# Optimization experiments

Measured on AMD Instinct MI355X. Metric: run time of the kernel, lower is better.

Reference implementation:

```python
import jax, jax.numpy as jnp
import numpy as np

B, N, DIM = 4, 2048, 768
HEADS, DH, DEPTH = 12, 64, 4
W = 35                     # hard-coded window size
P = DIM // 2               # window-embedding proj dim
V4 = DIM // 4              # window-embedding value dim
PB = DIM // 4              # dynamic pos-bias MLP width
FF = DIM * 4
NEG = float(np.finfo(np.float32).max)


def setup_inputs() -> dict:
    key = jax.random.key(0)
    ks = iter(jax.random.split(key, 32))
    r = lambda shape: jax.random.normal(next(ks), shape, jnp.float32) * 0.02
    return dict(
        x=jax.random.normal(next(ks), (B, N, DIM), jnp.float32),
        mask=jnp.zeros((B, N), bool),
        ln1_g=jnp.ones((DEPTH, DIM)), ln1_b=jnp.zeros((DEPTH, DIM)),
        qkv_W=r((DEPTH, DIM, 3 * HEADS * DH)),
        temp=jnp.full((DEPTH,), 15.5, jnp.float32),
        we_lin_W=r((DEPTH, DIM, P)), we_q_W=r((DEPTH, P, P)),
        we_k_W=r((DEPTH, DIM, P)), we_v_W=r((DEPTH, DIM, V4)),
        we_bos=jnp.zeros((DEPTH, V4)), we_scale=jnp.ones((DEPTH,)),
        out_W=r((DEPTH, DIM + V4, DIM)),
        ln2_g=jnp.ones((DEPTH, DIM)), ln2_b=jnp.zeros((DEPTH, DIM)),
        glu_W=r((DEPTH, DIM, 2 * FF)), glu_b=jnp.zeros((DEPTH, 2 * FF)),
        ffo_W=r((DEPTH, FF, DIM)), ffo_b=jnp.zeros((DEPTH, DIM)),
        pb_W1=r((1, PB)), pb_b1=jnp.zeros((PB,)),
        pb_W2=r((PB, PB)), pb_b2=jnp.zeros((PB,)),
        pb_W3=r((PB, HEADS)), pb_b3=jnp.zeros((HEADS,)),
    )


def _ln(x, g, b):
    m = x.mean(-1, keepdims=True)
    v = ((x - m) ** 2).mean(-1, keepdims=True)
    return (x - m) * jax.lax.rsqrt(v + 1e-5) * g + b


def _l2norm(t):
    # matches F.normalize(p=2, dim=-1): x / max(||x||, 1e-12)
    return t / jnp.maximum(jnp.linalg.norm(t, axis=-1, keepdims=True), 1e-12)


def _pos_bias(n, W1, b1, W2, b2, W3, b3):
    # DynamicPositionBias(dim=PB, depth=2): Linear->ReLU, Linear->ReLU, Linear
    pos = jnp.arange(-n + 1, n, dtype=jnp.float32)[:, None]          # (2n-1, 1)
    h = jax.nn.relu(pos @ W1 + b1)
    h = jax.nn.relu(h @ W2 + b2)
    out = h @ W3 + b3                                                # (2n-1, H)
    idx = jnp.arange(n)[:, None] - jnp.arange(n)[None, :] + n - 1    # (n, n)
    return jnp.transpose(out[idx], (2, 0, 1))                        # (H, n, n)


def _sinu(n, scale):
    # ScaledSinuEmbedding over proj dim P
    inv = 1.0 / (10000.0 ** (jnp.arange(0, P, 2, dtype=jnp.float32) / P))
    s = jnp.arange(n, dtype=jnp.float32)[:, None] * inv[None, :]
    return jnp.concatenate([jnp.sin(s), jnp.cos(s)], -1) * scale     # (n, P)


def _forward(x, mask, ln1_g, ln1_b, qkv_W, temp, we_lin_W, we_q_W, we_k_W,
             we_v_W, we_bos, we_scale, out_W, ln2_g, ln2_b, glu_W, glu_b,
             ffo_W, ffo_b, pb_W1, pb_b1, pb_W2, pb_b2, pb_W3, pb_b3):
    Bz, Nn, _ = x.shape
    pad = (-Nn) % W
    nw = (Nn + pad) // W
    bias = _pos_bias(W, pb_W1, pb_b1, pb_W2, pb_b2, pb_W3, pb_b3)    # (H, W, W)
    causal = jnp.triu(jnp.ones((W, W), bool), 1)
    mpad = jnp.concatenate([mask, jnp.ones((Bz, pad), bool)], 1).reshape(Bz, nw, W)
    valid = ~mpad                                                    # (B, w, n)
    amask = ~(valid[:, None, :, :, None] & valid[:, None, :, None, :]) | causal
    we_mask = mpad[:, :, None, :]                                    # (B, w, 1, n)
    lengths = jnp.maximum(valid.sum(-1), 1).astype(jnp.float32)[..., None, None]
    sinu35 = _sinu(W, 1.0)                                           # (W, P)

    for l in range(DEPTH):
        # ---- PreNorm + windowed cosine attention ----
        h = _ln(x, ln1_g[l], ln1_b[l])
        hp = jnp.concatenate([h, jnp.zeros((Bz, pad, DIM), h.dtype)], 1)
        hp = hp.reshape(Bz, nw, W, DIM)
        qkv = (hp @ qkv_W[l]).reshape(Bz, nw, W, HEADS, DH, 3)
        q, k, v = (jnp.transpose(qkv[..., i], (0, 3, 1, 2, 4)) for i in range(3))
        q, k = _l2norm(q), _l2norm(k)
        dots = jnp.einsum('bhwid,bhwjd->bhwij', q, k) * temp[l] + bias[None, :, None]
        dots = jnp.where(amask, -NEG, dots)
        attn = jax.nn.softmax(dots, axis=-1)
        o = jnp.einsum('bhwij,bhwjd->bhwid', attn, v)
        o = jnp.transpose(o, (0, 2, 3, 1, 4)).reshape(Bz, nw, W, HEADS * DH)
        # ---- window_embeddings: pooled prev-window embedding attention ----
        we = jnp.where(mpad[..., None], 0.0, o) @ we_lin_W[l]         # (B,w,n,P)
        we = jax.nn.relu(we.sum(-2, keepdims=True) / lengths)        # (B,w,1,P)
        wq = we @ we_q_W[l]
        k2 = o @ we_k_W[l] + sinu35 * we_scale[l]
        v2 = o @ we_v_W[l]
        d2 = jnp.einsum('bwid,bwjd->bwij', wq, k2) * (P ** -0.5)
        d2 = jnp.where(we_mask, -NEG, d2)
        o2 = jnp.einsum('bwij,bwjd->bwid', jax.nn.softmax(d2, -1), v2)  # (B,w,1,V4)
        bos = jnp.broadcast_to(we_bos[l], (Bz, 1, 1, V4))
        o2 = jnp.concatenate([bos, o2], 1)[:, :-1]                   # shift by one window
        o = jnp.concatenate([o, jnp.broadcast_to(o2, (Bz, nw, W, V4))], -1)
        o = (o @ out_W[l]).reshape(Bz, nw * W, DIM)[:, :Nn]
        x = x + o
        # ---- PreNorm + GLU feed-forward ----
        h2 = _ln(x, ln2_g[l], ln2_b[l])
        a, g = jnp.split(h2 @ glu_W[l] + glu_b[l], 2, axis=-1)
        x = x + ((a * jax.nn.silu(g)) @ ffo_W[l] + ffo_b[l])
    return x


def reference(x, mask, ln1_g, ln1_b, qkv_W, temp, we_lin_W, we_q_W, we_k_W,
              we_v_W, we_bos, we_scale, out_W, ln2_g, ln2_b, glu_W, glu_b,
              ffo_W, ffo_b, pb_W1, pb_b1, pb_W2, pb_b2, pb_W3, pb_b3):
    return _forward(x, mask, ln1_g, ln1_b, qkv_W, temp, we_lin_W, we_q_W,
                    we_k_W, we_v_W, we_bos, we_scale, out_W, ln2_g, ln2_b,
                    glu_W, glu_b, ffo_W, ffo_b, pb_W1, pb_b1, pb_W2, pb_b2,
                    pb_W3, pb_b3)
```

## Files before the change

kernel.cpp:

```cpp
#include <hip/hip_runtime.h>
#include <hip/hip_bf16.h>
#include <cstddef>
#include <cstdint>

#define B_ 4
#define N_ 2048
#define DIM_ 768
#define HEADS_ 12
#define DH_ 64
#define DEPTH_ 4
#define W_ 35
#define P_ 384
#define V4_ 192
#define FF_ 3072
#define NW_ 59
#define NPB_ (NW_*W_)
#define NTOK_ (B_*N_)
#define NWB_ (B_*NW_)
#define NTP_ (NWB_*W_)
#define NTPA_ 8448
#define NEG_ 3.402823466e+38f
#define QLD_ 65

typedef __bf16 bf16x8 __attribute__((ext_vector_type(8)));
typedef float  f32x4  __attribute__((ext_vector_type(4)));

#define GLOAD16(g, l) __builtin_amdgcn_global_load_lds( \
    (const __attribute__((address_space(1))) uint32_t*)(g), \
    (__attribute__((address_space(3))) uint32_t*)(l), 16, 0, 0)


__global__ __launch_bounds__(192) void posbias1_k(
    const float* __restrict__ W1, const float* __restrict__ b1,
    const float* __restrict__ W2, const float* __restrict__ b2,
    const float* __restrict__ W3, const float* __restrict__ b3,
    float* __restrict__ outk)
{
    __shared__ float h1[192];
    __shared__ float h2[192];
    int i = blockIdx.x;
    int tid = threadIdx.x;
    float pos = (float)(i - 34);
    h1[tid] = fmaxf(pos*W1[tid] + b1[tid], 0.f);
    __syncthreads();
    float s = b2[tid];
    for (int k=0;k<192;k++) s += h1[k]*W2[k*192+tid];
    h2[tid] = fmaxf(s, 0.f);
    __syncthreads();
    if (tid < 12){
        float o = b3[tid];
        for (int k=0;k<192;k++) o += h2[k]*W3[k*12+tid];
        outk[i*12+tid] = o;
    }
}

__global__ void posbias2_k(const float* __restrict__ outk, float* __restrict__ bias)
{
    int e = threadIdx.x + blockIdx.x*blockDim.x;
    if (e >= HEADS_*W_*W_) return;
    int h=e/(W_*W_); int rem=e%(W_*W_); int i=rem/W_; int j=rem%W_;
    bias[e] = outk[(i-j+W_-1)*12 + h];
}

__global__ void sinu_k(float* __restrict__ sinu)
{
    int i = blockIdx.x;
    int k = threadIdx.x;
    float inv = powf(10000.f, -(float)k/192.f);
    float s = (float)i * inv;
    sinu[i*P_ + k]       = sinf(s);
    sinu[i*P_ + 192 + k] = cosf(s);
}

__global__ void len_k(const unsigned char* __restrict__ mask, float* __restrict__ len)
{
    int bw = threadIdx.x + blockIdx.x*blockDim.x;
    if (bw >= NWB_) return;
    int b = bw / NW_, w = bw % NW_;
    int cnt = 0;
    for (int t=0;t<W_;t++){
        int g = w*W_ + t;
        if (g < N_ && mask[b*N_+g]==0) cnt++;
    }
    len[bw] = fmaxf((float)cnt, 1.f);
}

__global__ __launch_bounds__(256) void bosproj_k(
    const float* __restrict__ bos, const float* __restrict__ outW,
    float* __restrict__ bosp)
{
    int l = blockIdx.y;
    int c = blockIdx.x*256 + threadIdx.x;
    if (c >= DIM_) return;
    const float* W2 = outW + (size_t)l*(DIM_+V4_)*DIM_ + (size_t)DIM_*DIM_;
    const float* bl = bos + (size_t)l*V4_;
    float s = 0;
    for (int k=0;k<V4_;k++) s += bl[k]*W2[(size_t)k*DIM_ + c];
    bosp[(size_t)l*DIM_ + c] = s;
}

__global__ __launch_bounds__(256) void pack_k(
    const float* __restrict__ W, __bf16* __restrict__ Bp,
    int N, int Ncov, int Nld, size_t lsW, size_t lsB, int mode, int ncol0)
{
    int n = blockIdx.x*256 + threadIdx.x;
    int k8 = blockIdx.y, l = blockIdx.z;
    if (n >= Ncov) return;
    bf16x8 v;
    if (n < N){
        int sn = n;
        if (mode == 1){ int s = n/768, hd = n - s*768; sn = hd*3 + s; }
        else if (mode == 2){
            int bx = n >> 8, c = n & 255;
            int wcq = c >> 6, n2 = (c & 63) >> 4, lr2 = c & 15;
            int j = bx*128 + wcq*32 + ((n2>>1)<<4) + lr2;
            sn = (n2 & 1) ? FF_ + j : j;
        }
        const float* w = W + lsW*l + (size_t)k8*8*N + sn;
        #pragma unroll
        for (int e=0;e<8;e++) v[e] = (__bf16)w[(size_t)e*N];
    } else {
        #pragma unroll
        for (int e=0;e<8;e++) v[e] = (__bf16)0.f;
    }
    *(bf16x8*)(Bp + lsB*l + ((size_t)k8*Nld + ncol0 + n)*8) = v;
}

__global__ __launch_bounds__(256) void ln_k(
    const float* __restrict__ x, const float* __restrict__ g,
    const float* __restrict__ b, __bf16* __restrict__ out,
    const float* __restrict__ o2p, const float* __restrict__ bosp, int padded)
{
    int r = blockIdx.x;
    int tid = threadIdx.x;
    int lane = tid & 63, wave = tid >> 6;
    int row = r; bool real = true;
    if (padded){
        int bb = r / NPB_, n = r % NPB_;
        if (n >= N_) real = false;
        row = bb*N_ + n;
    }
    float v0=0,v1=0,v2=0;
    if (real){
        const float* xr = x + (size_t)row*DIM_;
        v0 = xr[tid]; v1 = xr[tid+256]; v2 = xr[tid+512];
        if (o2p){
            int bb = row / N_, nn = row % N_;
            int widx = nn / W_;
            const float* op = widx ? o2p + (size_t)(bb*NW_ + widx - 1)*DIM_
                                   : bosp;
            v0 += op[tid]; v1 += op[tid+256]; v2 += op[tid+512];
        }
    }
    float s1 = v0+v1+v2;
    float s2 = v0*v0+v1*v1+v2*v2;
    #pragma unroll
    for (int off=32; off; off>>=1){
        s1 += __shfl_xor(s1, off);
        s2 += __shfl_xor(s2, off);
    }
    __shared__ float a1[4], a2[4];
    if (lane==0){ a1[wave]=s1; a2[wave]=s2; }
    __syncthreads();
    s1 = a1[0]+a1[1]+a1[2]+a1[3];
    s2 = a2[0]+a2[1]+a2[2]+a2[3];
    float m   = s1 * (1.f/768.f);
    float var = s2 * (1.f/768.f) - m*m;
    float inv = rsqrtf(var + 1e-5f);
    __bf16* o = out + (size_t)r*DIM_;
    if (!real){ o[tid]=(__bf16)0.f; o[tid+256]=(__bf16)0.f; o[tid+512]=(__bf16)0.f; return; }
    o[tid]     = (__bf16)((v0-m)*inv*g[tid]     + b[tid]);
    o[tid+256] = (__bf16)((v1-m)*inv*g[tid+256] + b[tid+256]);
    o[tid+512] = (__bf16)((v2-m)*inv*g[tid+512] + b[tid+512]);
}

template<int EPI, bool DUAL, int BM>
__global__ __launch_bounds__(256) void mgemm_k(
    const __bf16* __restrict__ A, const __bf16* __restrict__ Bp,
    float* __restrict__ Cf, __bf16* __restrict__ Cb, float* __restrict__ Cf2,
    float* __restrict__ Cx,
    const float* __restrict__ bias, const float* __restrict__ extra,
    const float* __restrict__ scale_ptr,
    int M, int K, int Nc, int Nld, int Cld)
{
    constexpr int BN = DUAL ? 64 : 128;
    constexpr int RS = BM / 2;
    constexpr int MF = RS / 16;
    constexpr int NF = (BN/2) / 16;
    constexpr int AS = BM * 32;
    constexpr int BS = BN * 32;
    constexpr int ALD = BM / 64;
    constexpr int NL  = ALD + 2;
    __shared__ alignas(16) __bf16 As[3*AS];
    __shared__ alignas(16) __bf16 Bs[3*BS];
    __shared__ alignas(16) __bf16 Gs[DUAL ? 3*BS : 16];
    const int tid = threadIdx.x;
    const int lane = tid & 63, wave = tid >> 6;
    const int wr = wave >> 1, wc = wave & 1;
    const int m0 = blockIdx.y*BM;
    const int n0 = blockIdx.x*BN;
    const int lk = lane >> 4, lr = lane & 15;
    f32x4 acc[MF][NF] = {};
    f32x4 acc2[DUAL?MF:1][NF] = {};

    const __bf16* aP[ALD];
    int aO[ALD];
    #pragma unroll
    for (int q=0;q<ALD;q++){
        int i = tid + q*256;
        int r = i & (BM-1), k8 = i / BM;
        aP[q] = A + (size_t)(m0+r)*K + k8*8;
        aO[q] = i*8;
    }
    const __bf16* bP[2];
    int bO[2];
    if constexpr (!DUAL){
        #pragma unroll
        for (int q=0;q<2;q++){
            int i = tid + q*256;
            int n = i & 127, k8 = i >> 7;
            bP[q] = Bp + ((size_t)k8*Nld + n0 + n)*8;
            bO[q] = i*8;
        }
    } else {
        int n = tid & 63, k8 = tid >> 6;
        bP[0] = Bp + ((size_t)k8*Nld + n0 + n)*8;
        bP[1] = bP[0] + (size_t)FF_*8;
        bO[0] = tid*8;
        bO[1] = tid*8;
    }
    const size_t bStep = (size_t)Nld*32;

    auto stage = [&](int wb){
        #pragma unroll
        for (int q=0;q<ALD;q++)
            GLOAD16(aP[q], As + wb*AS + aO[q]);
        if constexpr (!DUAL){
            GLOAD16(bP[0], Bs + wb*BS + bO[0]);
            GLOAD16(bP[1], Bs + wb*BS + bO[1]);
        } else {
            GLOAD16(bP[0], Bs + wb*BS + bO[0]);
            GLOAD16(bP[1], Gs + wb*BS + bO[1]);
        }
        #pragma unroll
        for (int q=0;q<ALD;q++) aP[q] += 32;
        bP[0] += bStep; bP[1] += bStep;
    };

    const int nk = K >> 5;
    stage(0);
    stage(1);
    int rb = 0;
    for (int t = 0; t < nk; ++t){
        if (t == nk-1)              asm volatile("s_waitcnt vmcnt(0)" ::: "memory");
        else if constexpr (NL == 3) asm volatile("s_waitcnt vmcnt(3)" ::: "memory");
        else                        asm volatile("s_waitcnt vmcnt(4)" ::: "memory");
        __builtin_amdgcn_s_barrier();
        __builtin_amdgcn_sched_barrier(0);
        if (t + 2 < nk){
            int wb = rb + 2; if (wb >= 3) wb -= 3;
            stage(wb);
        }
        const __bf16* as = As + rb*AS + (size_t)(lk*BM + wr*RS + lr)*8;
        const __bf16* bs = Bs + rb*BS + (size_t)(lk*BN + wc*(BN/2) + lr)*8;
        bf16x8 af[MF], bfr[NF];
        #pragma unroll
        for (int m=0;m<MF;m++) af[m] = *(const bf16x8*)(as + m*128);
        #pragma unroll
        for (int n=0;n<NF;n++) bfr[n] = *(const bf16x8*)(bs + n*128);
        __builtin_amdgcn_s_setprio(1);
        #pragma unroll
        for (int m=0;m<MF;m++)
            #pragma unroll
            for (int n=0;n<NF;n++)
                acc[m][n] = __builtin_amdgcn_mfma_f32_16x16x32_bf16(af[m], bfr[n], acc[m][n], 0,0,0);
        if constexpr (DUAL){
            const __bf16* gs = Gs + rb*BS + (size_t)(lk*BN + wc*(BN/2) + lr)*8;
            bf16x8 gfr[NF];
            #pragma unroll
            for (int n=0;n<NF;n++) gfr[n] = *(const bf16x8*)(gs + n*128);
            #pragma unroll
            for (int m=0;m<MF;m++)
                #pragma unroll
                for (int n=0;n<NF;n++)
                    acc2[m][n] = __builtin_amdgcn_mfma_f32_16x16x32_bf16(af[m], gfr[n], acc2[m][n], 0,0,0);
        }
        __builtin_amdgcn_s_setprio(0);
        rb++; if (rb >= 3) rb = 0;
    }

    const int lq = lane >> 4;
    #pragma unroll
    for (int m=0;m<MF;m++){
        #pragma unroll
        for (int r=0;r<4;r++){
            int row = m0 + wr*RS + m*16 + lq*4 + r;
            if (row >= M) continue;
            #pragma unroll
            for (int n=0;n<NF;n++){
                int col = n0 + wc*(BN/2) + n*16 + lr;
                if (col >= Nc) continue;
                float v = acc[m][n][r];
                if (EPI==1){
                    Cb[(size_t)row*Cld + col] = (__bf16)v;
                } else if (EPI==3){
                    int bb = row / N_, nn = row % N_;
                    int widx = nn / W_;
                    const float* src = widx
                        ? extra + (size_t)(bb*NW_ + widx - 1)*DIM_
                        : scale_ptr;
                    Cf[(size_t)row*Cld + col] += v + bias[col] + src[col];
                } else if (EPI==4){
                    float a_ = v + bias[col];
                    float g_ = acc2[m][n][r] + bias[col + FF_];
                    Cb[(size_t)row*Cld + col] = (__bf16)(a_ * (g_ / (1.f + expf(-g_))));
                } else if (EPI==8){
                    if (col < P_){
                        int tt = (row % NPB_) % W_;
                        Cf[(size_t)row*P_ + col] = v + extra[tt*P_ + col]*scale_ptr[0];
                    } else if (col < 576){
                        Cf2[(size_t)row*V4_ + (col - P_)] = v;
                    } else {
                        int bb = row / NPB_, nn = row % NPB_;
                        if (nn < N_)
                            Cx[(size_t)(bb*N_ + nn)*DIM_ + (col - 576)] += v;
                    }
                }
            }
        }
    }
}

__global__ __launch_bounds__(512) void glu8_k(
    const __bf16* __restrict__ A, const __bf16* __restrict__ Bp,
    __bf16* __restrict__ Cb, const float* __restrict__ bias)
{
    __shared__ alignas(16) __bf16 As[2][16384];
    __shared__ alignas(16) __bf16 Bs[2][16384];
    const int tid = threadIdx.x;
    const int lane = tid & 63, wave = tid >> 6;
    const int wr = wave >> 2, wc = wave & 3;
    const int m0 = blockIdx.y << 8;
    const int n0p = blockIdx.x << 8;
    const int lk = lane >> 4, lr = lane & 15;
    f32x4 acc[8][4] = {};

    auto stageA = [&](int buf, int kt, int h){
        #pragma unroll
        for (int q=0;q<2;q++){
            int i = tid + q*512;
            int k8 = i >> 7, r = i & 127;
            GLOAD16(A + (size_t)(m0 + h*128 + r)*DIM_ + kt*64 + k8*8,
                    &As[buf][((size_t)k8*256 + h*128 + r)*8]);
        }
    };
    auto stageB = [&](int buf, int kt, int h){
        #pragma unroll
        for (int q=0;q<2;q++){
            int i = tid + q*512;
            int k8 = i >> 7, c = i & 127;
            GLOAD16(Bp + ((size_t)(kt*8 + k8)*6144 + n0p + h*128 + c)*8,
                    &Bs[buf][((size_t)k8*256 + h*128 + c)*8]);
        }
    };
    auto stageHalf = [&](int buf, int kt, int h){
        if (h < 2) stageA(buf, kt, h); else stageB(buf, kt, h-2);
    };

    #pragma unroll
    for (int h=0;h<4;h++) stageHalf(0, 0, h);
    #pragma unroll
    for (int h=0;h<4;h++) stageHalf(1, 1, h);
    asm volatile("s_waitcnt vmcnt(8)" ::: "memory");
    __builtin_amdgcn_s_barrier();
    __builtin_amdgcn_sched_barrier(0);

    const int niter = (DIM_/64) / 2;
    for (int j = 0; j < niter; ++j){
        #pragma unroll
        for (int p = 0; p < 8; ++p){
            const int g = p >> 2;
            const int q = p & 3;
            if (p == 0){
                if (j > 0) asm volatile("s_waitcnt vmcnt(0)" ::: "memory");
            } else if (p == 4){
                asm volatile("s_waitcnt vmcnt(0)" ::: "memory");
            }
            if (g == 0){
                if (j >= 1) stageHalf(1, 2*j+1, q);
            } else {
                if (2*j+2 < DIM_/64) stageHalf(0, 2*j+2, q);
            }
            const int rbase = wr*128 + (q&1)*64;
            const int cbase = wc*64  + ((q>>1))*32;
            const __bf16* as = &As[g][0];
            const __bf16* bs = &Bs[g][0];
            bf16x8 af[2][4], bfr[2][2];
            #pragma unroll
            for (int s=0;s<2;s++){
                #pragma unroll
                for (int m=0;m<4;m++)
                    af[s][m] = *(const bf16x8*)(as + ((size_t)((s*4+lk)*256 + rbase + m*16 + lr))*8);
                #pragma unroll
                for (int n=0;n<2;n++)
                    bfr[s][n] = *(const bf16x8*)(bs + ((size_t)((s*4+lk)*256 + cbase + n*16 + lr))*8);
            }
            __builtin_amdgcn_s_barrier();
            __builtin_amdgcn_sched_barrier(0);
            __builtin_amdgcn_s_setprio(1);
            #pragma unroll
            for (int s=0;s<2;s++)
                #pragma unroll
                for (int m=0;m<4;m++)
                    #pragma unroll
                    for (int n=0;n<2;n++)
                        acc[(q&1)*4 + m][(q>>1)*2 + n] =
                            __builtin_amdgcn_mfma_f32_16x16x32_bf16(
                                af[s][m], bfr[s][n],
                                acc[(q&1)*4 + m][(q>>1)*2 + n], 0,0,0);
            __builtin_amdgcn_s_setprio(0);
            __builtin_amdgcn_s_barrier();
            __builtin_amdgcn_sched_barrier(0);
        }
    }

    const int lq = lane >> 4;
    const int jc0 = (blockIdx.x << 7) + wc*32 + lr;
    #pragma unroll
    for (int mm=0;mm<8;mm++){
        int rowb = m0 + wr*128 + mm*16 + lq*4;
        #pragma unroll
        for (int hh=0; hh<2; hh++){
            int col = jc0 + hh*16;
            float ba = bias[col], bg = bias[col + FF_];
            #pragma unroll
            for (int r=0;r<4;r++){
                float a_ = acc[mm][hh*2][r] + ba;
                float g_ = acc[mm][hh*2+1][r] + bg;
                Cb[(size_t)(rowb + r)*FF_ + col] =
                    (__bf16)(a_ * (g_/(1.f + expf(-g_))));
            }
        }
    }
}

__global__ __launch_bounds__(256) void attn_k(
    const __bf16* __restrict__ qkv, const unsigned char* __restrict__ mask,
    const float* __restrict__ bias, const float* __restrict__ temp_p,
    __bf16* __restrict__ obuf, float* __restrict__ osum)
{
    int bid = blockIdx.x;
    int w = bid % NW_;
    int h = (bid / NW_) % HEADS_;
    int b = bid / (NW_*HEADS_);
    int tid = threadIdx.x;
    __shared__ float qs[W_*QLD_], ks[W_*QLD_], vs[W_*DH_];
    __shared__ float sc[W_*W_];
    __shared__ float osacc[4][64];
    __shared__ int vf[W_];
    int bw = b*NW_ + w;
    int rbase = bw*W_;
    for (int e=tid; e<W_*DH_; e+=256){
        int t=e>>6, d=e&63;
        size_t idx = (size_t)(rbase+t)*(3*DIM_) + h*DH_ + d;
        qs[t*QLD_+d]=(float)qkv[idx];
        ks[t*QLD_+d]=(float)qkv[idx+768];
        vs[e]=(float)qkv[idx+1536];
    }
    if (tid < W_){
        int g = w*W_ + tid;
        vf[tid] = (g < N_) && (mask[b*N_+g]==0);
    }
    __syncthreads();
    for (int e=tid; e<2*W_; e+=256){
        float* src = (e<W_)? qs : ks;
        int t = (e<W_)? e : e-W_;
        float s=0;
        for (int d=0;d<DH_;d++){ float v=src[t*QLD_+d]; s+=v*v; }
        float inv = 1.f / fmaxf(sqrtf(s), 1e-12f);
        for (int d=0;d<DH_;d++) src[t*QLD_+d] *= inv;
    }
    __syncthreads();
    float temp = temp_p[0];
    for (int e=tid; e<W_*W_; e+=256){
        int i=e/W_, j=e%W_;
        float s;
        if (!vf[i] || !vf[j] || j>i) s = -NEG_;
        else {
            float acc=0;
            for (int d=0;d<DH_;d++) acc += qs[i*QLD_+d]*ks[j*QLD_+d];
            s = acc*temp + bias[(h*W_+i)*W_+j];
        }
        sc[e]=s;
    }
    __syncthreads();
    if (tid < W_){
        int i=tid;
        float mx=-INFINITY;
        for (int j=0;j<W_;j++) mx=fmaxf(mx, sc[i*W_+j]);
        float sum=0;
        for (int j=0;j<W_;j++){ float e_=expf(sc[i*W_+j]-mx); sc[i*W_+j]=e_; sum+=e_; }
        float inv=1.f/sum;
        for (int j=0;j<W_;j++) sc[i*W_+j]*=inv;
    }
    __syncthreads();
    int wavei = tid >> 6, d = tid & 63;
    float psum = 0.f;
    for (int i = wavei; i < W_; i += 4){
        float s=0;
        for (int j=0;j<W_;j++) s += sc[i*W_+j]*vs[j*DH_+d];
        obuf[(size_t)(rbase+i)*DIM_ + h*DH_ + d] = (__bf16)s;
        if (vf[i]) psum += s;
    }
    osacc[wavei][d] = psum;
    __syncthreads();
    if (tid < 64)
        osum[(size_t)bw*DIM_ + h*DH_ + tid] =
            osacc[0][tid]+osacc[1][tid]+osacc[2][tid]+osacc[3][tid];
}

__global__ __launch_bounds__(384) void wefuse_k(
    const float* __restrict__ osum, const float* __restrict__ we_lin,
    const float* __restrict__ we_q, const float* __restrict__ k2,
    const float* __restrict__ v2, const unsigned char* __restrict__ mask,
    const float* __restrict__ len, const float* __restrict__ W2,
    float* __restrict__ o2p)
{
    int bw = blockIdx.x;
    int b = bw / NW_, w = bw % NW_;
    int tid = threadIdx.x;
    __shared__ float osr[768], werr[384], wqr[384], pp[W_], o2s[V4_];
    osr[tid]     = osum[(size_t)bw*DIM_ + tid];
    osr[tid+384] = osum[(size_t)bw*DIM_ + tid + 384];
    __syncthreads();
    float invlen = 1.f / len[bw];
    float s = 0;
    for (int k=0;k<768;k++) s += osr[k]*we_lin[(size_t)k*P_ + tid];
    werr[tid] = fmaxf(s*invlen, 0.f);
    __syncthreads();
    s = 0;
    for (int k=0;k<384;k++) s += werr[k]*we_q[(size_t)k*P_ + tid];
    wqr[tid] = s;
    __syncthreads();
    if (tid < W_){
        int g = w*W_ + tid;
        bool val = (g < N_) && (mask[b*N_+g]==0);
        float sv = -NEG_;
        if (val){
            float acc=0;
            const float* kr = k2 + (size_t)(bw*W_+tid)*P_;
            for (int c=0;c<P_;c++) acc += wqr[c]*kr[c];
            sv = acc * 0.05103103630798287f;
        }
        pp[tid]=sv;
    }
    __syncthreads();
    if (tid==0){
        float mx=-INFINITY;
        for (int j=0;j<W_;j++) mx=fmaxf(mx,pp[j]);
        float sum=0;
        for (int j=0;j<W_;j++){ float e=expf(pp[j]-mx); pp[j]=e; sum+=e; }
        float inv=1.f/sum;
        for (int j=0;j<W_;j++) pp[j]*=inv;
    }
    __syncthreads();
    if (tid < V4_){
        float sv=0;
        for (int j=0;j<W_;j++) sv += pp[j]*v2[(size_t)(bw*W_+j)*V4_ + tid];
        o2s[tid] = sv;
    }
    __syncthreads();
    #pragma unroll
    for (int c = tid; c < DIM_; c += 384){
        float s2 = 0;
        for (int k=0;k<V4_;k++) s2 += o2s[k]*W2[(size_t)k*DIM_ + c];
        o2p[(size_t)bw*DIM_ + c] = s2;
    }
}


extern "C" void kernel_launch(void* const* d_in, const int* in_sizes, int n_in,
                              void* d_out, int out_size, void* d_ws, size_t ws_size,
                              hipStream_t stream)
{
    const float* x       = (const float*)d_in[0];
    const unsigned char* mask = (const unsigned char*)d_in[1];
    const float* ln1_g   = (const float*)d_in[2];
    const float* ln1_b   = (const float*)d_in[3];
    const float* qkv_W   = (const float*)d_in[4];
    const float* temp    = (const float*)d_in[5];
    const float* we_lin_W= (const float*)d_in[6];
    const float* we_q_W  = (const float*)d_in[7];
    const float* we_k_W  = (const float*)d_in[8];
    const float* we_v_W  = (const float*)d_in[9];
    const float* we_bos  = (const float*)d_in[10];
    const float* we_scale= (const float*)d_in[11];
    const float* out_W   = (const float*)d_in[12];
    const float* ln2_g   = (const float*)d_in[13];
    const float* ln2_b   = (const float*)d_in[14];
    const float* glu_W   = (const float*)d_in[15];
    const float* glu_b   = (const float*)d_in[16];
    const float* ffo_W   = (const float*)d_in[17];
    const float* ffo_b   = (const float*)d_in[18];
    const float* pb_W1   = (const float*)d_in[19];
    const float* pb_b1   = (const float*)d_in[20];
    const float* pb_W2   = (const float*)d_in[21];
    const float* pb_b2   = (const float*)d_in[22];
    const float* pb_W3   = (const float*)d_in[23];
    const float* pb_b3   = (const float*)d_in[24];

    float* xc = (float*)d_out;

    char* p = (char*)d_ws;
    auto alloc = [&](size_t bytes)->char* {
        char* r = p; p += (bytes + 255) & ~(size_t)255; return r;
    };
    float* f_outk = (float*)alloc((size_t)69*12*4);
    float* f_bias = (float*)alloc((size_t)HEADS_*W_*W_*4);
    float* f_sinu = (float*)alloc((size_t)W_*P_*4);
    float* f_len  = (float*)alloc((size_t)NWB_*4);
    float* f_osum = (float*)alloc((size_t)NWB_*DIM_*4);
    float* f_o2p  = (float*)alloc((size_t)NWB_*DIM_*4);
    float* f_bosp = (float*)alloc((size_t)DEPTH_*DIM_*4);
    __bf16* w_qkv = (__bf16*)alloc((size_t)DEPTH_*96*2304*8*2);
    __bf16* w_kvo = (__bf16*)alloc((size_t)DEPTH_*96*1408*8*2);
    __bf16* w_glu = (__bf16*)alloc((size_t)DEPTH_*96*6144*8*2);
    __bf16* w_ffo = (__bf16*)alloc((size_t)DEPTH_*384*768*8*2);
    char* arena = p;
    __bf16* f_hpad = (__bf16*)alloc((size_t)NTPA_*DIM_*2);
    __bf16* f_qkvb = (__bf16*)alloc((size_t)NTP_*3*DIM_*2);
    __bf16* f_obuf = (__bf16*)alloc((size_t)NTPA_*DIM_*2);
    float*  f_k2   = (float*)alloc((size_t)NTP_*P_*4);
    float*  f_v2   = (float*)alloc((size_t)NTP_*V4_*4);
    __bf16* f_h2 = (__bf16*)arena;
    __bf16* f_ag = (__bf16*)(arena + (((size_t)NTOK_*DIM_*2 + 255) & ~(size_t)255));
    (void)ws_size; (void)in_sizes; (void)n_in; (void)out_size;

    hipMemcpyAsync(xc, x, (size_t)NTOK_*DIM_*sizeof(float),
                   hipMemcpyDeviceToDevice, stream);
    posbias1_k<<<69,192,0,stream>>>(pb_W1,pb_b1,pb_W2,pb_b2,pb_W3,pb_b3,f_outk);
    posbias2_k<<<(HEADS_*W_*W_+255)/256,256,0,stream>>>(f_outk, f_bias);
    sinu_k<<<W_,192,0,stream>>>(f_sinu);
    len_k<<<1,256,0,stream>>>(mask, f_len);
    bosproj_k<<<dim3(3,DEPTH_),256,0,stream>>>(we_bos, out_W, f_bosp);
    pack_k<<<dim3(9,96,DEPTH_),256,0,stream>>>(qkv_W, w_qkv, 2304, 2304, 2304,
        (size_t)768*2304, (size_t)96*2304*8, 1, 0);
    pack_k<<<dim3(2,96,DEPTH_),256,0,stream>>>(we_k_W, w_kvo, 384, 384, 1408,
        (size_t)768*384, (size_t)96*1408*8, 0, 0);
    pack_k<<<dim3(1,96,DEPTH_),256,0,stream>>>(we_v_W, w_kvo, 192, 192, 1408,
        (size_t)768*192, (size_t)96*1408*8, 0, 384);
    pack_k<<<dim3(4,96,DEPTH_),256,0,stream>>>(out_W, w_kvo, 768, 832, 1408,
        (size_t)960*768, (size_t)96*1408*8, 0, 576);
    pack_k<<<dim3(24,96,DEPTH_),256,0,stream>>>(glu_W, w_glu, 6144, 6144, 6144,
        (size_t)768*6144, (size_t)96*6144*8, 2, 0);
    pack_k<<<dim3(3,384,DEPTH_),256,0,stream>>>(ffo_W, w_ffo, 768, 768, 768,
        (size_t)3072*768, (size_t)384*768*8, 0, 0);

    for (int l=0;l<DEPTH_;l++){
        const float* bosp_l = f_bosp + (size_t)l*DIM_;
        ln_k<<<NTP_,256,0,stream>>>(xc, ln1_g+l*DIM_, ln1_b+l*DIM_, f_hpad,
            nullptr, nullptr, 1);
        mgemm_k<1,false,128><<<dim3(18,65),256,0,stream>>>(f_hpad,
            w_qkv + (size_t)l*96*2304*8, nullptr, f_qkvb, nullptr, nullptr,
            nullptr, nullptr, nullptr, NTP_, DIM_, 3*DIM_, 3*DIM_, 3*DIM_);
        attn_k<<<B_*HEADS_*NW_,256,0,stream>>>(f_qkvb, mask, f_bias, temp+l,
            f_obuf, f_osum);
        mgemm_k<8,false,64><<<dim3(11,130),256,0,stream>>>(f_obuf,
            w_kvo + (size_t)l*96*1408*8, f_k2, nullptr, f_v2, xc,
            nullptr, f_sinu, we_scale+l, NTP_, DIM_, 1344, 1408, 0);
        wefuse_k<<<NWB_,384,0,stream>>>(f_osum, we_lin_W + (size_t)l*DIM_*P_,
            we_q_W + (size_t)l*P_*P_, f_k2, f_v2, mask, f_len,
            out_W + (size_t)l*(DIM_+V4_)*DIM_ + (size_t)DIM_*DIM_, f_o2p);

        ln_k<<<NTOK_,256,0,stream>>>(xc, ln2_g+l*DIM_, ln2_b+l*DIM_, f_h2,
            f_o2p, bosp_l, 0);
        glu8_k<<<dim3(24,32),512,0,stream>>>(f_h2,
            w_glu + (size_t)l*96*6144*8, f_ag, glu_b + (size_t)l*2*FF_);
        mgemm_k<3,false,64><<<dim3(6,128),256,0,stream>>>(f_ag,
            w_ffo + (size_t)l*384*768*8, xc, nullptr, nullptr, nullptr,
            ffo_b + (size_t)l*DIM_, f_o2p, bosp_l,
            NTOK_, FF_, DIM_, DIM_, DIM_);
    }
}
```

Before: 1.987 ms.

## Restructure GLU GEMM to three-stage K=32 LDS ring buffer pipeline

Replaces the double-buffered K=64 tile pipeline in the GLU GEMM with a triple-buffered ring of K=32 stages, using precomputed pointer increments and one barrier per stage instead of two barriers per quarter. Each wave now loads its full 8x4 fragment set per stage and issues all MFMAs at once. The aim is to cut barrier and address overhead and keep loads further ahead of compute. The cost is more loop iterations with smaller K per stage, a different LDS access pattern that may bring bank conflicts, and slightly less LDS use.

Measured after the change: 2.094 ms, median of 2. 1.05x slower.

```diff
diff --git a/kernel.cpp b/kernel.cpp
--- a/kernel.cpp
+++ b/kernel.cpp
@@ -331,12 +331,12 @@
     }
 }
 
-__global__ __launch_bounds__(512) void glu8_k(
+__global__ __launch_bounds__(512) void glu3_k(
     const __bf16* __restrict__ A, const __bf16* __restrict__ Bp,
     __bf16* __restrict__ Cb, const float* __restrict__ bias)
 {
-    __shared__ alignas(16) __bf16 As[2][16384];
-    __shared__ alignas(16) __bf16 Bs[2][16384];
+    __shared__ alignas(16) __bf16 As[3*8192];
+    __shared__ alignas(16) __bf16 Bs[3*8192];
     const int tid = threadIdx.x;
     const int lane = tid & 63, wave = tid >> 6;
     const int wr = wave >> 2, wc = wave & 3;
@@ -345,83 +345,55 @@
     const int lk = lane >> 4, lr = lane & 15;
     f32x4 acc[8][4] = {};
 
-    auto stageA = [&](int buf, int kt, int h){
+    const __bf16* aP[2];
+    const __bf16* bP[2];
+    int aO[2];
+    #pragma unroll
+    for (int q=0;q<2;q++){
+        int i = tid + q*512;
+        int k8 = i >> 8, rc = i & 255;
+        aP[q] = A + (size_t)(m0 + rc)*DIM_ + k8*8;
+        bP[q] = Bp + ((size_t)k8*6144 + n0p + rc)*8;
+        aO[q] = i*8;
+    }
+    auto stage = [&](int wb){
         #pragma unroll
         for (int q=0;q<2;q++){
-            int i = tid + q*512;
-            int k8 = i >> 7, r = i & 127;
-            GLOAD16(A + (size_t)(m0 + h*128 + r)*DIM_ + kt*64 + k8*8,
-                    &As[buf][((size_t)k8*256 + h*128 + r)*8]);
-        }
+            GLOAD16(aP[q], As + wb*8192 + aO[q]);
+            GLOAD16(bP[q], Bs + wb*8192 + aO[q]);
+        }
+        #pragma unroll
+        for (int q=0;q<2;q++){ aP[q] += 32; bP[q] += (size_t)4*6144*8; }
     };
-    auto stageB = [&](int buf, int kt, int h){
-        #pragma unroll
-        for (int q=0;q<2;q++){
-            int i = tid + q*512;
-            int k8 = i >> 7, c = i & 127;
-            GLOAD16(Bp + ((size_t)(kt*8 + k8)*6144 + n0p + h*128 + c)*8,
-                    &Bs[buf][((size_t)k8*256 + h*128 + c)*8]);
-        }
-    };
-    auto stageHalf = [&](int buf, int kt, int h){
-        if (h < 2) stageA(buf, kt, h); else stageB(buf, kt, h-2);
-    };
-
-    #pragma unroll
-    for (int h=0;h<4;h++) stageHalf(0, 0, h);
-    #pragma unroll
-    for (int h=0;h<4;h++) stageHalf(1, 1, h);
-    asm volatile("s_waitcnt vmcnt(8)" ::: "memory");
-    __builtin_amdgcn_s_barrier();
-    __builtin_amdgcn_sched_barrier(0);
-
-    const int niter = (DIM_/64) / 2;
-    for (int j = 0; j < niter; ++j){
-        #pragma unroll
-        for (int p = 0; p < 8; ++p){
-            const int g = p >> 2;
-            const int q = p & 3;
-            if (p == 0){
-                if (j > 0) asm volatile("s_waitcnt vmcnt(0)" ::: "memory");
-            } else if (p == 4){
-                asm volatile("s_waitcnt vmcnt(0)" ::: "memory");
-            }
-            if (g == 0){
-                if (j >= 1) stageHalf(1, 2*j+1, q);
-            } else {
-                if (2*j+2 < DIM_/64) stageHalf(0, 2*j+2, q);
-            }
-            const int rbase = wr*128 + (q&1)*64;
-            const int cbase = wc*64  + ((q>>1))*32;
-            const __bf16* as = &As[g][0];
-            const __bf16* bs = &Bs[g][0];
-            bf16x8 af[2][4], bfr[2][2];
+
+    const int nk = DIM_ >> 5;
+    stage(0);
+    stage(1);
+    int rb = 0;
+    for (int t = 0; t < nk; ++t){
+        if (t == nk-1) asm volatile("s_waitcnt vmcnt(0)" ::: "memory");
+        else           asm volatile("s_waitcnt vmcnt(4)" ::: "memory");
+        __builtin_amdgcn_s_barrier();
+        __builtin_amdgcn_sched_barrier(0);
+        if (t + 2 < nk){
+            int wb = rb + 2; if (wb >= 3) wb -= 3;
+            stage(wb);
+        }
+        const __bf16* as = As + rb*8192 + (size_t)(lk*256 + wr*128 + lr)*8;
+        const __bf16* bs = Bs + rb*8192 + (size_t)(lk*256 + wc*64 + lr)*8;
+        bf16x8 af[8], bfr[4];
+        #pragma unroll
+        for (int m=0;m<8;m++) af[m] = *(const bf16x8*)(as + m*128);
+        #pragma unroll
+        for (int n=0;n<4;n++) bfr[n] = *(const bf16x8*)(bs + n*128);
+        __builtin_amdgcn_s_setprio(1);
+        #pragma unroll
+        for (int m=0;m<8;m++)
             #pragma unroll
-            for (int s=0;s<2;s++){
-                #pragma unroll
-                for (int m=0;m<4;m++)
-                    af[s][m] = *(const bf16x8*)(as + ((size_t)((s*4+lk)*256 + rbase + m*16 + lr))*8);
-                #pragma unroll
-                for (int n=0;n<2;n++)
-                    bfr[s][n] = *(const bf16x8*)(bs + ((size_t)((s*4+lk)*256 + cbase + n*16 + lr))*8);
-            }
-            __builtin_amdgcn_s_barrier();
-            __builtin_amdgcn_sched_barrier(0);
-            __builtin_amdgcn_s_setprio(1);
-            #pragma unroll
-            for (int s=0;s<2;s++)
-                #pragma unroll
-                for (int m=0;m<4;m++)
-                    #pragma unroll
-                    for (int n=0;n<2;n++)
-                        acc[(q&1)*4 + m][(q>>1)*2 + n] =
-                            __builtin_amdgcn_mfma_f32_16x16x32_bf16(
-                                af[s][m], bfr[s][n],
-                                acc[(q&1)*4 + m][(q>>1)*2 + n], 0,0,0);
-            __builtin_amdgcn_s_setprio(0);
-            __builtin_amdgcn_s_barrier();
-            __builtin_amdgcn_sched_barrier(0);
-        }
+            for (int n=0;n<4;n++)
+                acc[m][n] = __builtin_amdgcn_mfma_f32_16x16x32_bf16(af[m], bfr[n], acc[m][n], 0,0,0);
+        __builtin_amdgcn_s_setprio(0);
+        rb++; if (rb >= 3) rb = 0;
     }
 
     const int lq = lane >> 4;
@@ -674,7 +646,7 @@
 
         ln_k<<<NTOK_,256,0,stream>>>(xc, ln2_g+l*DIM_, ln2_b+l*DIM_, f_h2,
             f_o2p, bosp_l, 0);
-        glu8_k<<<dim3(24,32),512,0,stream>>>(f_h2,
+        glu3_k<<<dim3(24,32),512,0,stream>>>(f_h2,
             w_glu + (size_t)l*96*6144*8, f_ag, glu_b + (size_t)l*2*FF_);
         mgemm_k<3,false,64><<<dim3(6,128),256,0,stream>>>(f_ag,
             w_ffo + (size_t)l*384*768*8, xc, nullptr, nullptr, nullptr,
```
